# Kernel tuning notes

Measured on AMD Instinct MI355X. Metric: run time of the kernel, lower is better.

Reference implementation:

```python
import jax, jax.numpy as jnp
import numpy as np

NUM_NODES = 50000
NUM_EDGES = 600000
NUM_TYPES = 100
HIDDEN = 128
OUT = 64
NUM_GRAPHS = 256


def setup_inputs() -> dict:
    key = jax.random.key(0)
    ks = jax.random.split(key, 10)
    H = jax.random.randint(ks[0], (NUM_NODES, 1), 0, NUM_TYPES, dtype=jnp.int64)
    edge_index = jax.random.randint(ks[1], (2, NUM_EDGES), 0, NUM_NODES, dtype=jnp.int64)
    batch = jnp.sort(jax.random.randint(ks[2], (NUM_NODES,), 0, NUM_GRAPHS, dtype=jnp.int64))
    s = 1.0 / np.sqrt(HIDDEN)
    emb = jax.random.normal(ks[3], (NUM_TYPES, HIDDEN), dtype=jnp.float32)
    W1 = jax.random.uniform(ks[4], (HIDDEN, HIDDEN), jnp.float32, -s, s)
    b1 = jax.random.uniform(ks[5], (HIDDEN,), jnp.float32, -s, s)
    W2 = jax.random.uniform(ks[6], (HIDDEN, HIDDEN), jnp.float32, -s, s)
    b2 = jax.random.uniform(ks[7], (HIDDEN,), jnp.float32, -s, s)
    Wout = jax.random.uniform(ks[8], (OUT, HIDDEN), jnp.float32, -s, s)
    bout = jax.random.uniform(ks[9], (OUT,), jnp.float32, -s, s)
    return {"H": H, "edge_index": edge_index, "batch": batch,
            "emb": emb, "W1": W1, "b1": b1, "W2": W2, "b2": b2,
            "Wout": Wout, "bout": bout}


def reference(H, edge_index, batch, emb, W1, b1, W2, b2, Wout, bout):
    N = H.shape[0]
    # add self loops (pyg.utils.add_self_loops)
    ar = jnp.arange(N, dtype=edge_index.dtype)
    ei = jnp.concatenate([edge_index, jnp.stack([ar, ar])], axis=1)  # [2, E+N]
    row, col = ei[0], ei[1]
    # symmetric normalization deg^-1/2 (on rows, as in the source)
    deg = jax.ops.segment_sum(jnp.ones(row.shape[0], jnp.float32), row, num_segments=N)
    dinv = jnp.where(deg > 0, jax.lax.rsqrt(jnp.maximum(deg, 1.0)), 0.0)
    norm = (dinv[row] * dinv[col])[:, None]  # [E+N, 1]

    def gcn(x, W, b):
        h = x @ W.T + b                               # [N, hidden] GEMM
        msg = h[col] * norm                           # gather + scale
        h = jax.ops.segment_sum(msg, row, num_segments=N)  # scatter_add
        return jax.nn.relu(h)

    x = emb[H[:, 0]]            # embedding lookup, [N, hidden]
    x = gcn(x, W1, b1)
    x = gcn(x, W2, b2)
    # dropout in eval mode -> identity
    # global mean pool over graphs
    sums = jax.ops.segment_sum(x, batch, num_segments=NUM_GRAPHS)
    cnts = jax.ops.segment_sum(jnp.ones(N, jnp.float32), batch, num_segments=NUM_GRAPHS)
    pooled = sums / jnp.maximum(cnts, 1.0)[:, None]   # [G, hidden]
    out = pooled @ Wout.T + bout                      # [G, OUT]
    return jnp.squeeze(out)
```

## Files before the change

### kernel.cpp

```cpp
#include <hip/hip_runtime.h>

#define NN   50000
#define NE   600000
#define HID  128
#define NOUT_ 64
#define NG   256
#define NT   100
#define CAP  64

#define NN_P   50048
#define NTILES (NN_P / 16)
#define TPB    4
#define GEMM_GRID (NTILES / TPB)

typedef unsigned int u32;
typedef unsigned short u16;
typedef __attribute__((ext_vector_type(8))) short s16x8;
typedef __attribute__((ext_vector_type(4))) float f32x4;

static __device__ __forceinline__ float bflo(u32 u) { return __uint_as_float(u << 16); }
static __device__ __forceinline__ float bfhi(u32 u) { return __uint_as_float(u & 0xffff0000u); }
static __device__ __forceinline__ u32 pack2bf(float lo, float hi) {
  u32 ul = __float_as_uint(lo), uh = __float_as_uint(hi);
  ul = (ul + 0x7fffu + ((ul >> 16) & 1u)) >> 16;
  uh = (uh + 0x7fffu + ((uh >> 16) & 1u)) >> 16;
  return ul | (uh << 16);
}
static __device__ __forceinline__ u16 bf16rne(float f) {
  u32 u = __float_as_uint(f);
  u = (u + 0x7fffu + ((u >> 16) & 1u)) >> 16;
  return (u16)u;
}


#define NB_Z 49
#define NB_P 32
#define NB_W 64
#define NB_E 50
#define SETUP_GRID (NB_Z + NB_P + NB_W + NB_E)

static __global__ __launch_bounds__(256) void k_setup(
    int* __restrict__ cnts, float* __restrict__ poolSum,
    const float* __restrict__ W2, u16* __restrict__ whi, u16* __restrict__ wlo,
    const float* __restrict__ emb, const float* __restrict__ W1,
    const float* __restrict__ b1, u16* __restrict__ ewb) {
  __shared__ float er[2][HID];
  const int b = blockIdx.x, tid = threadIdx.x;
  if (b < NB_Z) {
    int i = b * 1024 + tid * 4;
    if (i < NN)
      *reinterpret_cast<int4*>(&cnts[i]) = make_int4(0, 0, 0, 0);
  } else if (b < NB_Z + NB_P) {
    int i = (b - NB_Z) * 1024 + tid * 4;
    *reinterpret_cast<float4*>(&poolSum[i]) = make_float4(0.f, 0.f, 0.f, 0.f);
  } else if (b < NB_Z + NB_P + NB_W) {
    int i = (b - NB_Z - NB_P) * 256 + tid;
    float w = W2[i];
    u16 hi = bf16rne(w);
    whi[i] = hi;
    wlo[i] = bf16rne(w - __uint_as_float(((u32)hi) << 16));
  } else {
    const int half = tid >> 7, o = tid & 127;
    const int t = (b - NB_Z - NB_P - NB_W) * 2 + half;
    er[half][o] = emb[(size_t)t * HID + o];
    __syncthreads();
    const float* wr = &W1[(size_t)o * HID];
    const float* e0 = er[half];
    float acc = 0.f;
#pragma unroll
    for (int k = 0; k < HID; k += 4) {
      float4 w = *reinterpret_cast<const float4*>(&wr[k]);
      acc += e0[k] * w.x + e0[k + 1] * w.y + e0[k + 2] * w.z + e0[k + 3] * w.w;
    }
    ewb[(size_t)t * HID + o] = bf16rne(acc + b1[o]);
  }
}


static __global__ void k_scatter(const int* __restrict__ row, const int* __restrict__ col,
                                 int* __restrict__ cnts, int* __restrict__ colIdx) {
  int e = blockIdx.x * 256 + threadIdx.x;
  if (e >= NE) return;
  int r = row[e];
  int slot = atomicAdd(&cnts[r], 1);
  if (slot < CAP) colIdx[(size_t)r * CAP + slot] = col[e];
}


static __global__ void k_hd(const int* __restrict__ cnts, const int* __restrict__ H,
                            float* __restrict__ dinv, int2* __restrict__ hd) {
  int i = blockIdx.x * 256 + threadIdx.x;
  if (i >= NN) return;
  float dv = rsqrtf((float)(cnts[i] + 1));
  dinv[i] = dv;
  hd[i] = make_int2(H[i], __float_as_int(dv));
}

static __global__ __launch_bounds__(256) void k_csr0(
    const int* __restrict__ cnts, const int* __restrict__ colIdx,
    const int2* __restrict__ hd, const u16* __restrict__ ewb,
    u16* __restrict__ x) {
  __shared__ u16 tl[NT * HID];
  const int tid = threadIdx.x;
  {
    const uint4* src = reinterpret_cast<const uint4*>(ewb);
    uint4* dst = reinterpret_cast<uint4*>(tl);
    for (int i = tid; i < NT * HID / 8; i += 256) dst[i] = src[i];
  }
  __syncthreads();

  const int node = blockIdx.x * 16 + (tid >> 4);
  if (node >= NN) return;
  const int lane = tid & 15;

  const int2 hn = hd[node];
  const float dn = __int_as_float(hn.y);
  float a[8];
  {
    uint4 v = *reinterpret_cast<const uint4*>(&tl[hn.x * HID + lane * 8]);
    a[0] = dn * bflo(v.x); a[1] = dn * bfhi(v.x);
    a[2] = dn * bflo(v.y); a[3] = dn * bfhi(v.y);
    a[4] = dn * bflo(v.z); a[5] = dn * bfhi(v.z);
    a[6] = dn * bflo(v.w); a[7] = dn * bfhi(v.w);
  }

  const int cnt = cnts[node];
  const int e = cnt < CAP ? cnt : CAP;
  const int* cp = &colIdx[(size_t)node * CAP];
  int i = 0;
  for (; i + 4 <= e; i += 4) {
    int2 h0 = hd[cp[i]], h1 = hd[cp[i + 1]];
    int2 h2 = hd[cp[i + 2]], h3 = hd[cp[i + 3]];
    uint4 w0 = *reinterpret_cast<const uint4*>(&tl[h0.x * HID + lane * 8]);
    uint4 w1 = *reinterpret_cast<const uint4*>(&tl[h1.x * HID + lane * 8]);
    uint4 w2 = *reinterpret_cast<const uint4*>(&tl[h2.x * HID + lane * 8]);
    uint4 w3 = *reinterpret_cast<const uint4*>(&tl[h3.x * HID + lane * 8]);
    float d0 = __int_as_float(h0.y), d1 = __int_as_float(h1.y);
    float d2 = __int_as_float(h2.y), d3 = __int_as_float(h3.y);
    a[0] += d0 * bflo(w0.x) + d1 * bflo(w1.x) + d2 * bflo(w2.x) + d3 * bflo(w3.x);
    a[1] += d0 * bfhi(w0.x) + d1 * bfhi(w1.x) + d2 * bfhi(w2.x) + d3 * bfhi(w3.x);
    a[2] += d0 * bflo(w0.y) + d1 * bflo(w1.y) + d2 * bflo(w2.y) + d3 * bflo(w3.y);
    a[3] += d0 * bfhi(w0.y) + d1 * bfhi(w1.y) + d2 * bfhi(w2.y) + d3 * bfhi(w3.y);
    a[4] += d0 * bflo(w0.z) + d1 * bflo(w1.z) + d2 * bflo(w2.z) + d3 * bflo(w3.z);
    a[5] += d0 * bfhi(w0.z) + d1 * bfhi(w1.z) + d2 * bfhi(w2.z) + d3 * bfhi(w3.z);
    a[6] += d0 * bflo(w0.w) + d1 * bflo(w1.w) + d2 * bflo(w2.w) + d3 * bflo(w3.w);
    a[7] += d0 * bfhi(w0.w) + d1 * bfhi(w1.w) + d2 * bfhi(w2.w) + d3 * bfhi(w3.w);
  }
  for (; i < e; ++i) {
    int2 h0 = hd[cp[i]];
    float d0 = __int_as_float(h0.y);
    uint4 w0 = *reinterpret_cast<const uint4*>(&tl[h0.x * HID + lane * 8]);
    a[0] += d0 * bflo(w0.x); a[1] += d0 * bfhi(w0.x);
    a[2] += d0 * bflo(w0.y); a[3] += d0 * bfhi(w0.y);
    a[4] += d0 * bflo(w0.z); a[5] += d0 * bfhi(w0.z);
    a[6] += d0 * bflo(w0.w); a[7] += d0 * bfhi(w0.w);
  }
#pragma unroll
  for (int k = 0; k < 8; ++k) a[k] = fmaxf(a[k] * dn, 0.f);
  uint4 o;
  o.x = pack2bf(a[0], a[1]); o.y = pack2bf(a[2], a[3]);
  o.z = pack2bf(a[4], a[5]); o.w = pack2bf(a[6], a[7]);
  reinterpret_cast<uint4*>(&x[(size_t)node * HID])[lane] = o;
}


static __global__ __launch_bounds__(256) void k_gemm(
    const u16* __restrict__ x,
    const u16* __restrict__ whi, const u16* __restrict__ wlo,
    const float* __restrict__ bias, const float* __restrict__ dinv,
    u16* __restrict__ g) {
  const int tid = threadIdx.x;
  const int wv = tid >> 6;
  const int l = tid & 63;
  const int l16 = l & 15, g4 = l >> 4;

  s16x8 wh[2][4], wl[2][4];
  float4 bb[2];
#pragma unroll
  for (int tt = 0; tt < 2; ++tt) {
    const int trow = (wv * 2 + tt) * 16 + l16;
#pragma unroll
    for (int s = 0; s < 4; ++s) {
      const int koff = s * 32 + g4 * 8;
      wh[tt][s] = *reinterpret_cast<const s16x8*>(&whi[(size_t)trow * HID + koff]);
      wl[tt][s] = *reinterpret_cast<const s16x8*>(&wlo[(size_t)trow * HID + koff]);
    }
    bb[tt] = *reinterpret_cast<const float4*>(&bias[(wv * 2 + tt) * 16 + g4 * 4]);
  }

  const int n0 = blockIdx.x * (TPB * 16) + l16;

  s16x8 xf[TPB][4];
  float dvv[TPB];
#pragma unroll
  for (int it = 0; it < TPB; ++it) {
    const int n = n0 + it * 16;
#pragma unroll
    for (int s = 0; s < 4; ++s)
      xf[it][s] = *reinterpret_cast<const s16x8*>(&x[(size_t)n * HID + s * 32 + g4 * 8]);
    dvv[it] = dinv[n];
  }

  f32x4 acc[TPB][2];
#pragma unroll
  for (int it = 0; it < TPB; ++it) {
    acc[it][0] = (f32x4){0.f, 0.f, 0.f, 0.f};
    acc[it][1] = (f32x4){0.f, 0.f, 0.f, 0.f};
  }
#pragma unroll
  for (int it = 0; it < TPB; ++it) {
#pragma unroll
    for (int s = 0; s < 4; ++s) {
#pragma unroll
      for (int tt = 0; tt < 2; ++tt) {
        acc[it][tt] = __builtin_amdgcn_mfma_f32_16x16x32_bf16(wh[tt][s], xf[it][s], acc[it][tt], 0, 0, 0);
        acc[it][tt] = __builtin_amdgcn_mfma_f32_16x16x32_bf16(wl[tt][s], xf[it][s], acc[it][tt], 0, 0, 0);
      }
    }
  }

#pragma unroll
  for (int it = 0; it < TPB; ++it) {
    const int n = n0 + it * 16;
#pragma unroll
    for (int tt = 0; tt < 2; ++tt) {
      const float v0 = (acc[it][tt][0] + bb[tt].x) * dvv[it];
      const float v1 = (acc[it][tt][1] + bb[tt].y) * dvv[it];
      const float v2 = (acc[it][tt][2] + bb[tt].z) * dvv[it];
      const float v3 = (acc[it][tt][3] + bb[tt].w) * dvv[it];
      *reinterpret_cast<uint2*>(&g[(size_t)n * HID + (wv * 2 + tt) * 16 + g4 * 4]) =
          make_uint2(pack2bf(v0, v1), pack2bf(v2, v3));
    }
  }
}


static __global__ __launch_bounds__(256) void k_csr_pool(
    const int* __restrict__ cnts, const int* __restrict__ colIdx,
    const u16* __restrict__ g, const float* __restrict__ dinv,
    const int* __restrict__ batch, float* __restrict__ poolSum) {
  __shared__ float xl[64][HID];
  __shared__ int bl[64];
  const int tid = threadIdx.x;
  const int nl = tid >> 2;
  const int j = tid & 3;
  const int node = blockIdx.x * 64 + nl;
  const u32* gw = (const u32*)g;

  float a[32];
  if (node < NN) {
    const u32* self = gw + (size_t)node * 64 + j * 16;
#pragma unroll
    for (int q = 0; q < 4; ++q) {
      uint4 v = *reinterpret_cast<const uint4*>(self + q * 4);
      a[q * 8 + 0] = bflo(v.x); a[q * 8 + 1] = bfhi(v.x);
      a[q * 8 + 2] = bflo(v.y); a[q * 8 + 3] = bfhi(v.y);
      a[q * 8 + 4] = bflo(v.z); a[q * 8 + 5] = bfhi(v.z);
      a[q * 8 + 6] = bflo(v.w); a[q * 8 + 7] = bfhi(v.w);
    }
    const int cnt = cnts[node];
    const int e = cnt < CAP ? cnt : CAP;
    const int* cp = &colIdx[(size_t)node * CAP];
    int i = 0;
    for (; i + 2 <= e; i += 2) {
      const u32* r0 = gw + (size_t)cp[i] * 64 + j * 16;
      const u32* r1 = gw + (size_t)cp[i + 1] * 64 + j * 16;
      uint4 v0[4], v1[4];
#pragma unroll
      for (int q = 0; q < 4; ++q) v0[q] = *reinterpret_cast<const uint4*>(r0 + q * 4);
#pragma unroll
      for (int q = 0; q < 4; ++q) v1[q] = *reinterpret_cast<const uint4*>(r1 + q * 4);
#pragma unroll
      for (int q = 0; q < 4; ++q) {
        a[q * 8 + 0] += bflo(v0[q].x) + bflo(v1[q].x);
        a[q * 8 + 1] += bfhi(v0[q].x) + bfhi(v1[q].x);
        a[q * 8 + 2] += bflo(v0[q].y) + bflo(v1[q].y);
        a[q * 8 + 3] += bfhi(v0[q].y) + bfhi(v1[q].y);
        a[q * 8 + 4] += bflo(v0[q].z) + bflo(v1[q].z);
        a[q * 8 + 5] += bfhi(v0[q].z) + bfhi(v1[q].z);
        a[q * 8 + 6] += bflo(v0[q].w) + bflo(v1[q].w);
        a[q * 8 + 7] += bfhi(v0[q].w) + bfhi(v1[q].w);
      }
    }
    if (i < e) {
      const u32* r0 = gw + (size_t)cp[i] * 64 + j * 16;
#pragma unroll
      for (int q = 0; q < 4; ++q) {
        uint4 v = *reinterpret_cast<const uint4*>(r0 + q * 4);
        a[q * 8 + 0] += bflo(v.x); a[q * 8 + 1] += bfhi(v.x);
        a[q * 8 + 2] += bflo(v.y); a[q * 8 + 3] += bfhi(v.y);
        a[q * 8 + 4] += bflo(v.z); a[q * 8 + 5] += bfhi(v.z);
        a[q * 8 + 6] += bflo(v.w); a[q * 8 + 7] += bfhi(v.w);
      }
    }
    const float d = dinv[node];
#pragma unroll
    for (int k = 0; k < 32; ++k) a[k] = fmaxf(a[k] * d, 0.f);
  } else {
#pragma unroll
    for (int k = 0; k < 32; ++k) a[k] = 0.f;
  }
#pragma unroll
  for (int k = 0; k < 32; ++k) xl[nl][j * 32 + k] = a[k];
  if (tid < 64) {
    int n2 = blockIdx.x * 64 + tid;
    bl[tid] = batch[n2 < NN ? n2 : NN - 1];
  }
  __syncthreads();

  const int d = tid & 127;
  const int half = tid >> 7;
  int gcur = bl[half * 32];
  float run = 0.f;
#pragma unroll 8
  for (int nd = half * 32; nd < half * 32 + 32; ++nd) {
    int gb = bl[nd];
    if (gb != gcur) {
      atomicAdd(&poolSum[gcur * HID + d], run);
      run = 0.f; gcur = gb;
    }
    run += xl[nd][d];
  }
  atomicAdd(&poolSum[gcur * HID + d], run);
}


static __device__ __forceinline__ int lb(const int* __restrict__ b, int n, int v) {
  int lo = 0, hi = n;
  while (lo < hi) { int m = (lo + hi) >> 1; if (b[m] < v) lo = m + 1; else hi = m; }
  return lo;
}

static __global__ __launch_bounds__(64) void k_head(
    const int* __restrict__ batch, const float* __restrict__ poolSum,
    const float* __restrict__ Wout, const float* __restrict__ bout,
    float* __restrict__ out) {
  const int g = blockIdx.x, o = threadIdx.x;
  const int s = lb(batch, NN, g);
  const int e = lb(batch, NN, g + 1);
  const float inv = 1.0f / fmaxf((float)(e - s), 1.0f);
  const float* ps = &poolSum[(size_t)g * HID];
  const float* wr = &Wout[(size_t)o * HID];
  float acc = 0.f;
#pragma unroll
  for (int k = 0; k < HID; k += 4) {
    float4 p = *reinterpret_cast<const float4*>(&ps[k]);
    float4 w = *reinterpret_cast<const float4*>(&wr[k]);
    acc += p.x * w.x + p.y * w.y + p.z * w.z + p.w * w.w;
  }
  out[g * NOUT_ + o] = acc * inv + bout[o];
}

extern "C" void kernel_launch(void* const* d_in, const int* in_sizes, int n_in,
                              void* d_out, int out_size, void* d_ws, size_t ws_size,
                              hipStream_t stream) {
  const int* H     = (const int*)d_in[0];
  const int* ei    = (const int*)d_in[1];
  const int* row   = ei;
  const int* col   = ei + NE;
  const int* batch = (const int*)d_in[2];
  const float* emb  = (const float*)d_in[3];
  const float* W1   = (const float*)d_in[4];
  const float* b1   = (const float*)d_in[5];
  const float* W2   = (const float*)d_in[6];
  const float* b2   = (const float*)d_in[7];
  const float* Wout = (const float*)d_in[8];
  const float* bout = (const float*)d_in[9];

  char* ws = (char*)d_ws;
  size_t off = 0;
  auto alloc = [&](size_t bytes) -> void* {
    void* p = (void*)(ws + off);
    off += (bytes + 255) & ~(size_t)255;
    return p;
  };
  int*   cnts    = (int*)alloc((size_t)NN * 4);
  int*   colIdx  = (int*)alloc((size_t)NN * CAP * 4);
  float* dinv    = (float*)alloc((size_t)NN_P * 4);
  int2*  hd      = (int2*)alloc((size_t)NN * 8);
  u16*   ewb     = (u16*)alloc((size_t)NT * HID * 2);
  u16*   whi     = (u16*)alloc((size_t)HID * HID * 2);
  u16*   wlo     = (u16*)alloc((size_t)HID * HID * 2);
  u16*   xbuf    = (u16*)alloc((size_t)NN_P * HID * 2);
  u16*   gbuf    = (u16*)alloc((size_t)NN_P * HID * 2);
  float* poolSum = (float*)alloc((size_t)NG * HID * 4);
  (void)ws_size; (void)in_sizes; (void)n_in; (void)out_size;

  const int nbE   = (NE + 255) / 256;
  const int nbN   = (NN + 255) / 256;
  const int nbC0  = (NN + 15) / 16;

  k_setup<<<SETUP_GRID, 256, 0, stream>>>(cnts, poolSum,
                                          W2, whi, wlo, emb, W1, b1, ewb);
  k_scatter<<<nbE, 256, 0, stream>>>(row, col, cnts, colIdx);
  k_hd<<<nbN, 256, 0, stream>>>(cnts, H, dinv, hd);

  k_csr0<<<nbC0, 256, 0, stream>>>(cnts, colIdx, hd, ewb, xbuf);
  k_gemm<<<GEMM_GRID, 256, 0, stream>>>(xbuf, whi, wlo, b2, dinv, gbuf);
  k_csr_pool<<<NN_P / 64, 256, 0, stream>>>(cnts, colIdx, gbuf, dinv, batch, poolSum);

  k_head<<<NG, NOUT_, 0, stream>>>(batch, poolSum, Wout, bout, (float*)d_out);
}
```

Measured before the change: 125.6 us.

## Pack node type with degree counter, drop k_hd kernel, precompute graph offsets

Each node's type index is stored in the upper bits of its atomic degree counter, and dinv is recomputed on the fly with rsqrt wherever it is needed. This removes the separate k_hd kernel and the hd/dinv buffers, and halves the gathered neighbour metadata from int2 to a single int. The setup kernel also writes per-graph start offsets so the head kernel no longer binary-searches `batch`, and the pooling shared buffer is padded to avoid LDS bank conflicts. In exchange, rsqrt is recomputed per edge. Correctness now assumes node degree stays below 256.

```diff
diff --git a/kernel.cpp b/kernel.cpp
--- a/kernel.cpp
+++ b/kernel.cpp
@@ -31,6 +31,9 @@
   u = (u + 0x7fffu + ((u >> 16) & 1u)) >> 16;
   return (u16)u;
 }
+static __device__ __forceinline__ float dv_of(int m) {
+  return rsqrtf((float)((m & 255) + 1));
+}
 
 
 #define NB_Z 49
@@ -40,16 +43,27 @@
 #define SETUP_GRID (NB_Z + NB_P + NB_W + NB_E)
 
 static __global__ __launch_bounds__(256) void k_setup(
-    int* __restrict__ cnts, float* __restrict__ poolSum,
+    int* __restrict__ mcnt, float* __restrict__ poolSum, int* __restrict__ gs,
+    const int* __restrict__ batch, const int* __restrict__ H,
     const float* __restrict__ W2, u16* __restrict__ whi, u16* __restrict__ wlo,
     const float* __restrict__ emb, const float* __restrict__ W1,
     const float* __restrict__ b1, u16* __restrict__ ewb) {
   __shared__ float er[2][HID];
   const int b = blockIdx.x, tid = threadIdx.x;
   if (b < NB_Z) {
-    int i = b * 1024 + tid * 4;
-    if (i < NN)
-      *reinterpret_cast<int4*>(&cnts[i]) = make_int4(0, 0, 0, 0);
+    int i0 = b * 1024 + tid * 4;
+#pragma unroll
+    for (int q = 0; q < 4; ++q) {
+      int idx = i0 + q;
+      if (idx < NN) {
+        mcnt[idx] = H[idx] << 8;
+        int b0 = batch[idx];
+        int b1 = (idx + 1 < NN) ? batch[idx + 1] : NG;
+        for (int g = b0 + 1; g <= b1; ++g) gs[g] = idx + 1;
+        if (idx == 0)
+          for (int g = 0; g <= b0; ++g) gs[g] = 0;
+      }
+    }
   } else if (b < NB_Z + NB_P) {
     int i = (b - NB_Z) * 1024 + tid * 4;
     *reinterpret_cast<float4*>(&poolSum[i]) = make_float4(0.f, 0.f, 0.f, 0.f);
@@ -78,28 +92,17 @@
 
 
 static __global__ void k_scatter(const int* __restrict__ row, const int* __restrict__ col,
-                                 int* __restrict__ cnts, int* __restrict__ colIdx) {
+                                 int* __restrict__ mcnt, int* __restrict__ colIdx) {
   int e = blockIdx.x * 256 + threadIdx.x;
   if (e >= NE) return;
   int r = row[e];
-  int slot = atomicAdd(&cnts[r], 1);
+  int slot = atomicAdd(&mcnt[r], 1) & 255;
   if (slot < CAP) colIdx[(size_t)r * CAP + slot] = col[e];
 }
 
-
-static __global__ void k_hd(const int* __restrict__ cnts, const int* __restrict__ H,
-                            float* __restrict__ dinv, int2* __restrict__ hd) {
-  int i = blockIdx.x * 256 + threadIdx.x;
-  if (i >= NN) return;
-  float dv = rsqrtf((float)(cnts[i] + 1));
-  dinv[i] = dv;
-  hd[i] = make_int2(H[i], __float_as_int(dv));
-}
-
 static __global__ __launch_bounds__(256) void k_csr0(
-    const int* __restrict__ cnts, const int* __restrict__ colIdx,
-    const int2* __restrict__ hd, const u16* __restrict__ ewb,
-    u16* __restrict__ x) {
+    const int* __restrict__ mcnt, const int* __restrict__ colIdx,
+    const u16* __restrict__ ewb, u16* __restrict__ x) {
   __shared__ u16 tl[NT * HID];
   const int tid = threadIdx.x;
   {
@@ -113,30 +116,29 @@
   if (node >= NN) return;
   const int lane = tid & 15;
 
-  const int2 hn = hd[node];
-  const float dn = __int_as_float(hn.y);
+  const int mn = mcnt[node];
+  const float dn = dv_of(mn);
   float a[8];
   {
-    uint4 v = *reinterpret_cast<const uint4*>(&tl[hn.x * HID + lane * 8]);
+    uint4 v = *reinterpret_cast<const uint4*>(&tl[(mn >> 8) * HID + lane * 8]);
     a[0] = dn * bflo(v.x); a[1] = dn * bfhi(v.x);
     a[2] = dn * bflo(v.y); a[3] = dn * bfhi(v.y);
     a[4] = dn * bflo(v.z); a[5] = dn * bfhi(v.z);
     a[6] = dn * bflo(v.w); a[7] = dn * bfhi(v.w);
   }
 
-  const int cnt = cnts[node];
+  const int cnt = mn & 255;
   const int e = cnt < CAP ? cnt : CAP;
   const int* cp = &colIdx[(size_t)node * CAP];
   int i = 0;
   for (; i + 4 <= e; i += 4) {
-    int2 h0 = hd[cp[i]], h1 = hd[cp[i + 1]];
-    int2 h2 = hd[cp[i + 2]], h3 = hd[cp[i + 3]];
-    uint4 w0 = *reinterpret_cast<const uint4*>(&tl[h0.x * HID + lane * 8]);
-    uint4 w1 = *reinterpret_cast<const uint4*>(&tl[h1.x * HID + lane * 8]);
-    uint4 w2 = *reinterpret_cast<const uint4*>(&tl[h2.x * HID + lane * 8]);
-    uint4 w3 = *reinterpret_cast<const uint4*>(&tl[h3.x * HID + lane * 8]);
-    float d0 = __int_as_float(h0.y), d1 = __int_as_float(h1.y);
-    float d2 = __int_as_float(h2.y), d3 = __int_as_float(h3.y);
+    int m0 = mcnt[cp[i]], m1 = mcnt[cp[i + 1]];
+    int m2 = mcnt[cp[i + 2]], m3 = mcnt[cp[i + 3]];
+    uint4 w0 = *reinterpret_cast<const uint4*>(&tl[(m0 >> 8) * HID + lane * 8]);
+    uint4 w1 = *reinterpret_cast<const uint4*>(&tl[(m1 >> 8) * HID + lane * 8]);
+    uint4 w2 = *reinterpret_cast<const uint4*>(&tl[(m2 >> 8) * HID + lane * 8]);
+    uint4 w3 = *reinterpret_cast<const uint4*>(&tl[(m3 >> 8) * HID + lane * 8]);
+    float d0 = dv_of(m0), d1 = dv_of(m1), d2 = dv_of(m2), d3 = dv_of(m3);
     a[0] += d0 * bflo(w0.x) + d1 * bflo(w1.x) + d2 * bflo(w2.x) + d3 * bflo(w3.x);
     a[1] += d0 * bfhi(w0.x) + d1 * bfhi(w1.x) + d2 * bfhi(w2.x) + d3 * bfhi(w3.x);
     a[2] += d0 * bflo(w0.y) + d1 * bflo(w1.y) + d2 * bflo(w2.y) + d3 * bflo(w3.y);
@@ -147,9 +149,9 @@
     a[7] += d0 * bfhi(w0.w) + d1 * bfhi(w1.w) + d2 * bfhi(w2.w) + d3 * bfhi(w3.w);
   }
   for (; i < e; ++i) {
-    int2 h0 = hd[cp[i]];
-    float d0 = __int_as_float(h0.y);
-    uint4 w0 = *reinterpret_cast<const uint4*>(&tl[h0.x * HID + lane * 8]);
+    int m0 = mcnt[cp[i]];
+    float d0 = dv_of(m0);
+    uint4 w0 = *reinterpret_cast<const uint4*>(&tl[(m0 >> 8) * HID + lane * 8]);
     a[0] += d0 * bflo(w0.x); a[1] += d0 * bfhi(w0.x);
     a[2] += d0 * bflo(w0.y); a[3] += d0 * bfhi(w0.y);
     a[4] += d0 * bflo(w0.z); a[5] += d0 * bfhi(w0.z);
@@ -167,7 +169,7 @@
 static __global__ __launch_bounds__(256) void k_gemm(
     const u16* __restrict__ x,
     const u16* __restrict__ whi, const u16* __restrict__ wlo,
-    const float* __restrict__ bias, const float* __restrict__ dinv,
+    const float* __restrict__ bias, const int* __restrict__ mcnt,
     u16* __restrict__ g) {
   const int tid = threadIdx.x;
   const int wv = tid >> 6;
@@ -198,7 +200,7 @@
 #pragma unroll
     for (int s = 0; s < 4; ++s)
       xf[it][s] = *reinterpret_cast<const s16x8*>(&x[(size_t)n * HID + s * 32 + g4 * 8]);
-    dvv[it] = dinv[n];
+    dvv[it] = dv_of(mcnt[n]);
   }
 
   f32x4 acc[TPB][2];
@@ -235,11 +237,13 @@
 }
 
 
+#define XLB (64 * 33 + 8)
+
 static __global__ __launch_bounds__(256) void k_csr_pool(
-    const int* __restrict__ cnts, const int* __restrict__ colIdx,
-    const u16* __restrict__ g, const float* __restrict__ dinv,
-    const int* __restrict__ batch, float* __restrict__ poolSum) {
-  __shared__ float xl[64][HID];
+    const int* __restrict__ mcnt, const int* __restrict__ colIdx,
+    const u16* __restrict__ g, const int* __restrict__ batch,
+    float* __restrict__ poolSum) {
+  __shared__ float XL[4 * XLB];
   __shared__ int bl[64];
   const int tid = threadIdx.x;
   const int nl = tid >> 2;
@@ -258,7 +262,8 @@
       a[q * 8 + 4] = bflo(v.z); a[q * 8 + 5] = bfhi(v.z);
       a[q * 8 + 6] = bflo(v.w); a[q * 8 + 7] = bfhi(v.w);
     }
-    const int cnt = cnts[node];
+    const int mn = mcnt[node];
+    const int cnt = mn & 255;
     const int e = cnt < CAP ? cnt : CAP;
     const int* cp = &colIdx[(size_t)node * CAP];
     int i = 0;
@@ -293,7 +298,7 @@
         a[q * 8 + 6] += bflo(v.w); a[q * 8 + 7] += bfhi(v.w);
       }
     }
-    const float d = dinv[node];
+    const float d = dv_of(mn);
 #pragma unroll
     for (int k = 0; k < 32; ++k) a[k] = fmaxf(a[k] * d, 0.f);
   } else {
@@ -301,7 +306,7 @@
     for (int k = 0; k < 32; ++k) a[k] = 0.f;
   }
 #pragma unroll
-  for (int k = 0; k < 32; ++k) xl[nl][j * 32 + k] = a[k];
+  for (int k = 0; k < 32; ++k) XL[j * XLB + nl * 33 + k] = a[k];
   if (tid < 64) {
     int n2 = blockIdx.x * 64 + tid;
     bl[tid] = batch[n2 < NN ? n2 : NN - 1];
@@ -310,6 +315,8 @@
 
   const int d = tid & 127;
   const int half = tid >> 7;
+  const int jb = (d >> 5) * XLB;
+  const int c = d & 31;
   int gcur = bl[half * 32];
   float run = 0.f;
 #pragma unroll 8
@@ -319,25 +326,19 @@
       atomicAdd(&poolSum[gcur * HID + d], run);
       run = 0.f; gcur = gb;
     }
-    run += xl[nd][d];
+    run += XL[jb + nd * 33 + c];
   }
   atomicAdd(&poolSum[gcur * HID + d], run);
 }
 
 
-static __device__ __forceinline__ int lb(const int* __restrict__ b, int n, int v) {
-  int lo = 0, hi = n;
-  while (lo < hi) { int m = (lo + hi) >> 1; if (b[m] < v) lo = m + 1; else hi = m; }
-  return lo;
-}
-
 static __global__ __launch_bounds__(64) void k_head(
-    const int* __restrict__ batch, const float* __restrict__ poolSum,
+    const int* __restrict__ gs, const float* __restrict__ poolSum,
     const float* __restrict__ Wout, const float* __restrict__ bout,
     float* __restrict__ out) {
   const int g = blockIdx.x, o = threadIdx.x;
-  const int s = lb(batch, NN, g);
-  const int e = lb(batch, NN, g + 1);
+  const int s = gs[g];
+  const int e = gs[g + 1];
   const float inv = 1.0f / fmaxf((float)(e - s), 1.0f);
   const float* ps = &poolSum[(size_t)g * HID];
   const float* wr = &Wout[(size_t)o * HID];
@@ -374,10 +375,9 @@
     off += (bytes + 255) & ~(size_t)255;
     return p;
   };
-  int*   cnts    = (int*)alloc((size_t)NN * 4);
+  int*   mcnt    = (int*)alloc((size_t)NN * 4);
   int*   colIdx  = (int*)alloc((size_t)NN * CAP * 4);
-  float* dinv    = (float*)alloc((size_t)NN_P * 4);
-  int2*  hd      = (int2*)alloc((size_t)NN * 8);
+  int*   gs      = (int*)alloc((size_t)(NG + 1) * 4);
   u16*   ewb     = (u16*)alloc((size_t)NT * HID * 2);
   u16*   whi     = (u16*)alloc((size_t)HID * HID * 2);
   u16*   wlo     = (u16*)alloc((size_t)HID * HID * 2);
@@ -387,17 +387,15 @@
   (void)ws_size; (void)in_sizes; (void)n_in; (void)out_size;
 
   const int nbE   = (NE + 255) / 256;
-  const int nbN   = (NN + 255) / 256;
   const int nbC0  = (NN + 15) / 16;
 
-  k_setup<<<SETUP_GRID, 256, 0, stream>>>(cnts, poolSum,
+  k_setup<<<SETUP_GRID, 256, 0, stream>>>(mcnt, poolSum, gs, batch, H,
                                           W2, whi, wlo, emb, W1, b1, ewb);
-  k_scatter<<<nbE, 256, 0, stream>>>(row, col, cnts, colIdx);
-  k_hd<<<nbN, 256, 0, stream>>>(cnts, H, dinv, hd);
-
-  k_csr0<<<nbC0, 256, 0, stream>>>(cnts, colIdx, hd, ewb, xbuf);
-  k_gemm<<<GEMM_GRID, 256, 0, stream>>>(xbuf, whi, wlo, b2, dinv, gbuf);
-  k_csr_pool<<<NN_P / 64, 256, 0, stream>>>(cnts, colIdx, gbuf, dinv, batch, poolSum);
-
-  k_head<<<NG, NOUT_, 0, stream>>>(batch, poolSum, Wout, bout, (float*)d_out);
-}
+  k_scatter<<<nbE, 256, 0, stream>>>(row, col, mcnt, colIdx);
+
+  k_csr0<<<nbC0, 256, 0, stream>>>(mcnt, colIdx, ewb, xbuf);
+  k_gemm<<<GEMM_GRID, 256, 0, stream>>>(xbuf, whi, wlo, b2, mcnt, gbuf);
+  k_csr_pool<<<NN_P / 64, 256, 0, stream>>>(mcnt, colIdx, gbuf, batch, poolSum);
+
+  k_head<<<NG, NOUT_, 0, stream>>>(gs, poolSum, Wout, bout, (float*)d_out);
+}
```

After: 120.1 us. -4.4%, faster.
